# Performance work log

Measured on AMD Instinct MI355X. Metric: run time of the kernel, lower is better.

The kernel has to match this reference:

```python
import jax, jax.numpy as jnp
import numpy as np

N = 10000
E = 160000
F_IN = 2000
HID = 128
NC = 5


def setup_inputs() -> dict:
    key = jax.random.key(0)
    ks = jax.random.split(key, 16)
    s = 0.05
    nrm = lambda k, shape: jax.random.normal(k, shape, jnp.float32) * s
    return {
        "x": jax.random.normal(ks[0], (N, F_IN), jnp.float32),
        "edge_index": jax.random.randint(ks[1], (2, E), 0, N),
        # GATConv 1: in=F_IN, out=HID, heads=6, concat=False
        "W_gat1": nrm(ks[2], (F_IN, 6 * HID)), "a_src1": nrm(ks[3], (6, HID)),
        "a_dst1": nrm(ks[4], (6, HID)), "b_gat1": jnp.zeros(HID, jnp.float32),
        # GCNConv 1
        "W_gcn1": nrm(ks[5], (HID, HID)), "b_gcn1": jnp.zeros(HID, jnp.float32),
        # GATConv 2: heads=4
        "W_gat2": nrm(ks[6], (HID, 4 * HID)), "a_src2": nrm(ks[7], (4, HID)),
        "a_dst2": nrm(ks[8], (4, HID)), "b_gat2": jnp.zeros(HID, jnp.float32),
        # GCNConv 2: out=HID//2
        "W_gcn2": nrm(ks[9], (HID, HID // 2)), "b_gcn2": jnp.zeros(HID // 2, jnp.float32),
        # skip projection / fusion
        "W_skip": nrm(ks[10], (F_IN, HID // 2)), "b_skip": jnp.zeros(HID // 2, jnp.float32),
        "W_fuse": nrm(ks[11], (HID + HID // 2, HID // 2)), "b_fuse": jnp.zeros(HID // 2, jnp.float32),
        # classifier MLP
        "W_c1": nrm(ks[12], (HID // 2, HID // 4)), "b_c1": jnp.zeros(HID // 4, jnp.float32),
        "W_c2": nrm(ks[13], (HID // 4, HID // 8)), "b_c2": jnp.zeros(HID // 8, jnp.float32),
        "W_c3": nrm(ks[14], (HID // 8, NC)), "b_c3": jnp.zeros(NC, jnp.float32),
        # LayerNorms
        "g1": jnp.ones(HID, jnp.float32), "be1": jnp.zeros(HID, jnp.float32),
        "g2": jnp.ones(HID, jnp.float32), "be2": jnp.zeros(HID, jnp.float32),
        "g3": jnp.ones(HID // 2, jnp.float32), "be3": jnp.zeros(HID // 2, jnp.float32),
    }


def layer_norm(x, g, b, eps=1e-5):
    mu = jnp.mean(x, axis=-1, keepdims=True)
    var = jnp.var(x, axis=-1, keepdims=True)
    return (x - mu) * jax.lax.rsqrt(var + eps) * g + b


def gat_conv(x, src, dst, W, a_src, a_dst, b, n):
    # PyG GATConv with concat=False (head-mean). Eval mode -> no attn dropout.
    H, C = a_src.shape
    h = (x @ W).reshape(-1, H, C)                      # [N,H,C]
    alpha = (h * a_src).sum(-1)[src] + (h * a_dst).sum(-1)[dst]  # [E,H]
    alpha = jax.nn.leaky_relu(alpha, 0.2)
    m = jax.ops.segment_max(alpha, dst, num_segments=n)
    e = jnp.exp(alpha - m[dst])
    w = e / jax.ops.segment_sum(e, dst, num_segments=n)[dst]     # segment softmax over incoming edges
    out = jax.ops.segment_sum(h[src] * w[:, :, None], dst, num_segments=n)  # [N,H,C]
    return out.mean(axis=1) + b


def gcn_conv(x, src, dst, W, b, n):
    deg = jax.ops.segment_sum(jnp.ones_like(dst, x.dtype), dst, num_segments=n)
    dinv = jnp.where(deg > 0, deg ** -0.5, 0.0)
    msg = (x @ W)[src] * (dinv[src] * dinv[dst])[:, None]
    return jax.ops.segment_sum(msg, dst, num_segments=n) + b


def reference(x, edge_index, W_gat1, a_src1, a_dst1, b_gat1, W_gcn1, b_gcn1,
              W_gat2, a_src2, a_dst2, b_gat2, W_gcn2, b_gcn2,
              W_skip, b_skip, W_fuse, b_fuse, W_c1, b_c1, W_c2, b_c2, W_c3, b_c3,
              g1, be1, g2, be2, g3, be3):
    n = x.shape[0]
    loop = jnp.arange(n, dtype=edge_index.dtype)
    src = jnp.concatenate([edge_index[0], loop])  # add_self_loops
    dst = jnp.concatenate([edge_index[1], loop])

    x1_gat = jax.nn.relu(layer_norm(gat_conv(x, src, dst, W_gat1, a_src1, a_dst1, b_gat1, n), g1, be1))
    x1_gcn = jax.nn.relu(gcn_conv(x1_gat, src, dst, W_gcn1, b_gcn1, n))
    x2_gat = jax.nn.relu(layer_norm(gat_conv(x1_gcn, src, dst, W_gat2, a_src2, a_dst2, b_gat2, n), g2, be2))
    x2_gcn = jax.nn.relu(gcn_conv(x2_gat, src, dst, W_gcn2, b_gcn2, n))

    skip = jax.nn.relu(x @ W_skip + b_skip)
    fused = jax.nn.relu(jnp.concatenate([x1_gcn, x2_gcn], axis=1) @ W_fuse + b_fuse)
    final = layer_norm(fused + skip, g3, be3)

    h = jax.nn.relu(final @ W_c1 + b_c1)
    h = jax.nn.relu(h @ W_c2 + b_c2)
    return h @ W_c3 + b_c3
```

## Files before the change

### kernel.cpp

```cpp
#include <hip/hip_runtime.h>
#include <cstdint>
#include <cstddef>

#define NN 10000
#define NE 160000
#define ET (NE + NN)
#define FIN 2000
#define MPAD 10112
#define KPAD 2048
#define NPAD 896

typedef __bf16 bf16x8 __attribute__((ext_vector_type(8)));
typedef __bf16 bf16x4 __attribute__((ext_vector_type(4)));
typedef float  f32x4  __attribute__((ext_vector_type(4)));

#define GLL(src, dst) __builtin_amdgcn_global_load_lds( \
    (const __attribute__((address_space(1))) void*)(src), \
    (__attribute__((address_space(3))) void*)(dst), 16, 0, 0)

__device__ __forceinline__ void edge_sd(const int* ei, int e, int& s, int& d) {
    if (e < NE) { s = ei[e]; d = ei[NE + e]; }
    else        { s = e - NE; d = e - NE; }
}

__global__ __launch_bounds__(1024)
void scan_kernel(const int* deg, int* rowstart, float* dinv) {
    __shared__ int wsum[16];
    const int T = 1024;
    int chunk = (NN + T - 1) / T;
    int t = threadIdx.x;
    int begin = t * chunk;
    int end = begin + chunk; if (end > NN) end = NN;
    if (begin > NN) begin = NN;
    int s = 0;
    for (int i = begin; i < end; i++) s += deg[i];
    int inc = s;
#pragma unroll
    for (int off = 1; off < 64; off <<= 1) {
        int u = __shfl_up(inc, off);
        if ((t & 63) >= off) inc += u;
    }
    if ((t & 63) == 63) wsum[t >> 6] = inc;
    __syncthreads();
    int woff = 0;
    for (int wv = 0; wv < (t >> 6); wv++) woff += wsum[wv];
    int run = woff + inc - s;
    for (int i = begin; i < end; i++) {
        rowstart[i] = run; run += deg[i];
        int dg = deg[i];
        dinv[i] = dg > 0 ? rsqrtf((float)dg) : 0.f;
    }
    if (end == NN) rowstart[NN] = run;
}

__global__ void scatter_kernel(const int* ei, const int* rowstart, int* cursor,
                               int* csr_src) {
    int e = blockIdx.x * blockDim.x + threadIdx.x;
    if (e >= ET) return;
    int s, d; edge_sd(ei, e, s, d);
    int pos = atomicAdd(&cursor[d], 1);
    csr_src[rowstart[d] + pos] = s;
}

#define NBX (158 * 8)
#define NW1 (NPAD * KPAD / 8)
#define NWT (NW1 + 512 * 128 / 8)
#define NWT2 (NWT + 2048 + 1024)
#define WBLK ((NWT2 + 255) / 256)
#define EB 665
__global__ void conv_kernel(const float* __restrict__ x, __bf16* __restrict__ xb,
                            const float* __restrict__ Wg, const float* __restrict__ Ws,
                            const float* __restrict__ W2,
                            const float* __restrict__ Wg1, const float* __restrict__ Wg2,
                            __bf16* __restrict__ wt, __bf16* __restrict__ w2t,
                            __bf16* __restrict__ wgcn1s, __bf16* __restrict__ wgcn2s,
                            const int* __restrict__ ei, int* __restrict__ deg) {
    __shared__ __bf16 ls[16384];
    int bid = blockIdx.x;
    int tid = threadIdx.x;
    if (bid < NBX) {
        int rt = bid >> 3, kb = bid & 7;
        const int lane16 = tid & 15;
        const int ksl = lane16 >> 2;
        const int p0 = (lane16 & 3) * 2;
        const int rbase = tid >> 4;
        const int kg0 = kb * 256 + lane16 * 16;
        const int rsw_x = (p0 & 6) ^ ksl;
#pragma unroll
        for (int pass = 0; pass < 4; pass++) {
            int r = pass * 16 + rbase;
            int row = rt * 64 + r;
            bf16x8 v0, v1;
#pragma unroll
            for (int j = 0; j < 4; j++) {
                int k = kg0 + j * 4;
                f32x4 f;
                if (row < NN && k + 3 < FIN)
                    f = *(const f32x4*)(x + (size_t)row * FIN + k);
                else
                    f = (f32x4){0.f, 0.f, 0.f, 0.f};
                int o = (j & 1) * 4;
                if (j < 2) {
                    v0[o] = (__bf16)f[0]; v0[o+1] = (__bf16)f[1];
                    v0[o+2] = (__bf16)f[2]; v0[o+3] = (__bf16)f[3];
                } else {
                    v1[o] = (__bf16)f[0]; v1[o+1] = (__bf16)f[1];
                    v1[o+2] = (__bf16)f[2]; v1[o+3] = (__bf16)f[3];
                }
            }
            int rsw = r ^ rsw_x;
            *(bf16x8*)(ls + (((ksl * 8 + p0) * 64 + rsw) * 8))     = v0;
            *(bf16x8*)(ls + (((ksl * 8 + p0 + 1) * 64 + rsw) * 8)) = v1;
        }
        __syncthreads();
        size_t cbase = ((size_t)rt * 32 + kb * 4) * 512;
#pragma unroll
        for (int i = 0; i < 8; i++) {
            int g = i * 256 + tid;
            int ksl2 = g >> 9, rem = g & 511;
            int p = rem >> 6, rr = rem & 63;
            int rsw = rr ^ ((p & 6) ^ ksl2);
            bf16x8 v = *(const bf16x8*)(ls + (((ksl2 * 8 + p) * 64 + rsw) * 8));
            *(bf16x8*)(xb + (cbase + (size_t)ksl2 * 512 + (p * 64 + rr)) * 8) = v;
        }
    } else if (bid < NBX + WBLK) {
        int g = (bid - NBX) * 256 + tid;
        if (g < NW1) {
            int r = g & 127, p = (g >> 7) & 7, ks = (g >> 10) & 31, ct = g >> 15;
            int n = ct * 128 + r;
            int k0 = ks * 64 + p * 8;
            bf16x8 o;
#pragma unroll
            for (int j = 0; j < 8; j++) {
                int k = k0 + j;
                float v = 0.f;
                if (k < FIN) {
                    if (n < 768)      v = Wg[(size_t)k * 768 + n];
                    else if (n < 832) v = Ws[(size_t)k * 64 + (n - 768)];
                }
                o[j] = (__bf16)v;
            }
            *(bf16x8*)(wt + (size_t)g * 8) = o;
        } else if (g < NWT) {
            int g2 = g - NW1;
            int c = g2 & 2047;
            int ct = g2 >> 11;
            int p = c >> 7, r = c & 127;
            int n = ct * 128 + r;
            int k0 = p * 8;
            bf16x8 o;
#pragma unroll
            for (int j = 0; j < 8; j++)
                o[j] = (__bf16)W2[(size_t)(k0 + j) * 512 + n];
            *(bf16x8*)(w2t + (size_t)g2 * 8) = o;
        } else if (g < NWT + 2048) {
            int g3 = g - NWT;
            int p = g3 >> 7, r = g3 & 127;
            bf16x8 o;
#pragma unroll
            for (int j = 0; j < 8; j++)
                o[j] = (__bf16)Wg1[(size_t)(p * 8 + j) * 128 + r];
            *(bf16x8*)(wgcn1s + (size_t)g3 * 8) = o;
        } else if (g < NWT2) {
            int g4 = g - NWT - 2048;
            int p = g4 >> 6, r = g4 & 63;
            bf16x8 o;
#pragma unroll
            for (int j = 0; j < 8; j++)
                o[j] = (__bf16)Wg2[(size_t)(p * 8 + j) * 64 + r];
            *(bf16x8*)(wgcn2s + (size_t)g4 * 8) = o;
        }
    } else {
        int e = (bid - NBX - WBLK) * 256 + tid;
        if (e < ET) {
            int s, d; edge_sd(ei, e, s, d);
            atomicAdd(&deg[d], 1);
        }
    }
}

__global__ __launch_bounds__(512)
void mfma_gemm1_kernel(const __bf16* __restrict__ xb, const __bf16* __restrict__ wt,
                       const float* __restrict__ a_src1, const float* __restrict__ a_dst1,
                       __bf16* __restrict__ h1b, float* __restrict__ skippre,
                       float* __restrict__ asrc, float* __restrict__ adst) {
    __shared__ __bf16 As[8192];
    __shared__ __bf16 Bs[8192];
    __shared__ float sA[128], sD[128];
    __shared__ float asd[256];
    int b = blockIdx.x;
    int xcd = b & 7, j = b >> 3;
    int jq = j / 7;
    int rt = xcd + 8 * jq;
    int ct = j - 7 * jq;
    if (rt >= MPAD / 128) return;
    const int bi = rt * 128;
    const int bn = ct * 128;

    const int tid = threadIdx.x;
    const int lane = tid & 63;
    const int w = tid >> 6;
    const int wm = w >> 1;
    const int wn = w & 1;
    const int q = lane >> 4, m16 = lane & 15;

    if (tid < 128) { sA[tid] = 0.f; sD[tid] = 0.f; }
    if (ct < 6) {
        if (tid < 128)      asd[tid] = a_src1[ct * 128 + tid];
        else if (tid < 256) asd[tid] = a_dst1[ct * 128 + (tid - 128)];
    }

    f32x4 acc[2][4] = {};

    for (int ks = 0; ks < KPAD / 64; ks++) {
        const size_t slabA = ((size_t)(rt * 2) * 32 + ks) * 512;
        const size_t slabB = ((size_t)ct * 32 + ks) * 1024;
#pragma unroll
        for (int i = 0; i < 2; i++) {
            int seg = i * 8 + w;
            int p = seg >> 1, h = seg & 1;
            GLL(xb + (slabA + (size_t)h * 16384 + p * 64 + lane) * 8,
                As + seg * 512);
        }
#pragma unroll
        for (int i = 0; i < 2; i++) {
            int seg = i * 8 + w;
            GLL(wt + (slabB + seg * 64 + lane) * 8, Bs + seg * 512);
        }
        __syncthreads();

#pragma unroll
        for (int kk = 0; kk < 2; kk++) {
            const int pb = kk * 4 + q;
            bf16x8 af[2], bfr[4];
#pragma unroll
            for (int mt = 0; mt < 2; mt++)
                af[mt] = *(const bf16x8*)(As + (pb * 128 + wm * 32 + mt * 16 + m16) * 8);
#pragma unroll
            for (int nt = 0; nt < 4; nt++)
                bfr[nt] = *(const bf16x8*)(Bs + (pb * 128 + wn * 64 + nt * 16 + m16) * 8);
#pragma unroll
            for (int mt = 0; mt < 2; mt++)
#pragma unroll
                for (int nt = 0; nt < 4; nt++)
                    acc[mt][nt] = __builtin_amdgcn_mfma_f32_16x16x32_bf16(af[mt], bfr[nt], acc[mt][nt], 0, 0, 0);
        }
        __syncthreads();
    }

#pragma unroll
    for (int mt = 0; mt < 2; mt++) {
#pragma unroll
        for (int r = 0; r < 4; r++) {
            int rowl = wm * 32 + mt * 16 + q * 4 + r;
            int row = bi + rowl;
            float ps = 0.f, pd = 0.f;
#pragma unroll
            for (int nt = 0; nt < 4; nt++) {
                int coll = wn * 64 + nt * 16 + m16;
                int col = bn + coll;
                float v = acc[mt][nt][r];
                if (ct < 6) { ps += v * asd[coll]; pd += v * asd[128 + coll]; }
                if (row < NN) {
                    if (col < 768)      h1b[(size_t)row * 768 + col] = (__bf16)v;
                    else if (col < 832) skippre[(size_t)row * 64 + (col - 768)] = v;
                }
            }
            if (ct < 6) {
#pragma unroll
                for (int off = 1; off < 16; off <<= 1) {
                    ps += __shfl_xor(ps, off);
                    pd += __shfl_xor(pd, off);
                }
                if (m16 == 0) { atomicAdd(&sA[rowl], ps); atomicAdd(&sD[rowl], pd); }
            }
        }
    }
    if (ct < 6) {
        __syncthreads();
        if (tid < 128) {
            int row = bi + tid;
            if (row < NN) { asrc[row * 6 + ct] = sA[tid]; adst[row * 6 + ct] = sD[tid]; }
        }
    }
}

__global__ __launch_bounds__(256)
void mfma_gemm2_kernel(const __bf16* __restrict__ A, const __bf16* __restrict__ B,
                       const float* __restrict__ a_src2, const float* __restrict__ a_dst2,
                       __bf16* __restrict__ h2b,
                       float* __restrict__ asrc, float* __restrict__ adst) {
    __shared__ __bf16 As[4096];
    __shared__ __bf16 Bs[8192];
    __shared__ float sA[64], sD[64];
    __shared__ float asd[256];
    const int rt = blockIdx.y, ct = blockIdx.x;
    const int bi = rt * 64, bn = ct * 128;
    const int tid = threadIdx.x, lane = tid & 63, w = tid >> 6;
    const int wm = w >> 1, wn = w & 1;
    const int q = lane >> 4, m16 = lane & 15;

    if (tid < 64) { sA[tid] = 0.f; sD[tid] = 0.f; }
    if (tid < 128) asd[tid] = a_src2[ct * 128 + tid];
    else           asd[tid] = a_dst2[ct * 128 + (tid - 128)];

    f32x4 acc[2][4] = {};

    for (int ks = 0; ks < 2; ks++) {
        const size_t slabA = (size_t)rt * 1024 + ks * 512;
        const size_t slabB = (size_t)ct * 2048 + ks * 1024;
#pragma unroll
        for (int i = 0; i < 2; i++) {
            int seg = i * 4 + w;
            GLL(A + (slabA + seg * 64 + lane) * 8, As + seg * 512);
        }
#pragma unroll
        for (int i = 0; i < 4; i++) {
            int seg = i * 4 + w;
            GLL(B + (slabB + seg * 64 + lane) * 8, Bs + seg * 512);
        }
        __syncthreads();

#pragma unroll
        for (int kk = 0; kk < 2; kk++) {
            const int pb = kk * 4 + q;
            bf16x8 af[2], bfr[4];
#pragma unroll
            for (int mt = 0; mt < 2; mt++)
                af[mt] = *(const bf16x8*)(As + (pb * 64 + wm * 32 + mt * 16 + m16) * 8);
#pragma unroll
            for (int nt = 0; nt < 4; nt++)
                bfr[nt] = *(const bf16x8*)(Bs + (pb * 128 + wn * 64 + nt * 16 + m16) * 8);
#pragma unroll
            for (int mt = 0; mt < 2; mt++)
#pragma unroll
                for (int nt = 0; nt < 4; nt++)
                    acc[mt][nt] = __builtin_amdgcn_mfma_f32_16x16x32_bf16(af[mt], bfr[nt], acc[mt][nt], 0, 0, 0);
        }
        __syncthreads();
    }

#pragma unroll
    for (int mt = 0; mt < 2; mt++) {
#pragma unroll
        for (int r = 0; r < 4; r++) {
            int rowl = wm * 32 + mt * 16 + q * 4 + r;
            int row = bi + rowl;
            float ps = 0.f, pd = 0.f;
#pragma unroll
            for (int nt = 0; nt < 4; nt++) {
                int coll = wn * 64 + nt * 16 + m16;
                float v = acc[mt][nt][r];
                ps += v * asd[coll]; pd += v * asd[128 + coll];
                if (row < NN) h2b[(size_t)row * 512 + bn + coll] = (__bf16)v;
            }
#pragma unroll
            for (int off = 1; off < 16; off <<= 1) {
                ps += __shfl_xor(ps, off);
                pd += __shfl_xor(pd, off);
            }
            if (m16 == 0) { atomicAdd(&sA[rowl], ps); atomicAdd(&sD[rowl], pd); }
        }
    }
    __syncthreads();
    if (tid < 64) {
        int row = bi + tid;
        if (row < NN) { asrc[row * 4 + ct] = sA[tid]; adst[row * 4 + ct] = sD[tid]; }
    }
}

template<int NT>
__global__ __launch_bounds__(256)
void mfma_gcn_kernel(const __bf16* __restrict__ A, const __bf16* __restrict__ B,
                     __bf16* __restrict__ Cb) {
    __shared__ __bf16 As[4096];
    __shared__ __bf16 Bs[NT * 64];
    const int rt = blockIdx.x;
    const int bi = rt * 64;
    const int tid = threadIdx.x, lane = tid & 63, w = tid >> 6;
    const int q = lane >> 4, m16 = lane & 15;
    constexpr int MT = (NT == 128) ? 2 : 1;
    constexpr int MSPAN = (NT == 128) ? 32 : 16;
    const int wm = (NT == 128) ? (w >> 1) : w;
    const int wn = (NT == 128) ? (w & 1) : 0;

    f32x4 acc[MT][4] = {};

    for (int ks = 0; ks < 2; ks++) {
        const size_t slabA = (size_t)rt * 1024 + ks * 512;
        const size_t slabB = (size_t)ks * (NT * 8);
#pragma unroll
        for (int i = 0; i < 2; i++) {
            int seg = i * 4 + w;
            GLL(A + (slabA + seg * 64 + lane) * 8, As + seg * 512);
        }
#pragma unroll
        for (int i = 0; i < NT / 32; i++) {
            int seg = i * 4 + w;
            GLL(B + (slabB + (size_t)seg * 64 + lane) * 8, Bs + seg * 512);
        }
        __syncthreads();

#pragma unroll
        for (int kk = 0; kk < 2; kk++) {
            const int pb = kk * 4 + q;
            bf16x8 af[MT], bfr[4];
#pragma unroll
            for (int mt = 0; mt < MT; mt++)
                af[mt] = *(const bf16x8*)(As + (pb * 64 + wm * MSPAN + mt * 16 + m16) * 8);
#pragma unroll
            for (int nt = 0; nt < 4; nt++)
                bfr[nt] = *(const bf16x8*)(Bs + (pb * NT + wn * 64 + nt * 16 + m16) * 8);
#pragma unroll
            for (int mt = 0; mt < MT; mt++)
#pragma unroll
                for (int nt = 0; nt < 4; nt++)
                    acc[mt][nt] = __builtin_amdgcn_mfma_f32_16x16x32_bf16(af[mt], bfr[nt], acc[mt][nt], 0, 0, 0);
        }
        __syncthreads();
    }

#pragma unroll
    for (int mt = 0; mt < MT; mt++) {
#pragma unroll
        for (int r = 0; r < 4; r++) {
            int row = bi + wm * MSPAN + mt * 16 + q * 4 + r;
            if (row >= NN) continue;
#pragma unroll
            for (int nt = 0; nt < 4; nt++) {
                int col = wn * 64 + nt * 16 + m16;
                Cb[(size_t)row * NT + col] = (__bf16)acc[mt][nt][r];
            }
        }
    }
}

template<int H>
__global__ void gat_agg_kernel(const __bf16* __restrict__ hb,
                               const float* __restrict__ asrc,
                               const float* __restrict__ adst,
                               const int* __restrict__ rowstart,
                               const int* __restrict__ csr_src,
                               const float* __restrict__ bias,
                               const float* __restrict__ gamma,
                               const float* __restrict__ beta,
                               __bf16* __restrict__ outs) {
    constexpr int CH = H * 128;
    constexpr int CAP = 128;
    int n = blockIdx.x;
    int t = threadIdx.x;
    int w = t >> 6, l = t & 63;
    __shared__ float invden[H];
    __shared__ float denp[256];
    __shared__ int   srcs[CAP];
    __shared__ float evs[CAP * H];
    __shared__ float sm[4 * CH];
    __shared__ float red[8];

    int s0 = rowstart[n];
    int deg = rowstart[n + 1] - s0;
    int degc = deg < CAP ? deg : CAP;
    float adst_n = (l < H) ? adst[n * H + l] : 0.f;

    if (t < degc) srcs[t] = csr_src[s0 + t];
    __syncthreads();

    const int h0 = l >> 4;
    const int h1i = 4 + (l >> 5);
    const int i0 = w, i1 = w + 4;
    const bool has0 = i0 < degc, has1 = i1 < degc;
    bf16x8 pg0, pg1; bf16x4 pe0, pe1;
    if (has0) {
        const __bf16* hp = hb + (size_t)srcs[i0] * CH;
        pg0 = *(const bf16x8*)(hp + l * 8);
        if (H == 6) pe0 = *(const bf16x4*)(hp + 512 + l * 4);
    }
    if (has1) {
        const __bf16* hp = hb + (size_t)srcs[i1] * CH;
        pg1 = *(const bf16x8*)(hp + l * 8);
        if (H == 6) pe1 = *(const bf16x4*)(hp + 512 + l * 4);
    }

    const int eh = t >> 3;
    const int hh1 = t & 7;
    float adst_h = (hh1 < H) ? adst[n * H + hh1] : 0.f;
    float dloc = 0.f;
    for (int base = 0; base < deg; base += 32) {
        int idx = base + eh;
        if (idx < deg && hh1 < H) {
            int src = (idx < CAP) ? srcs[idx] : csr_src[s0 + idx];
            float al = asrc[src * H + hh1] + adst_h;
            al = al >= 0.f ? al : 0.2f * al;
            float ev = __expf(al);
            dloc += ev;
            if (idx < CAP) evs[idx * H + hh1] = ev;
        }
    }
    denp[t] = dloc;
    __syncthreads();
    if (t < H) {
        float s = 0.f;
#pragma unroll
        for (int g = 0; g < 32; g++) s += denp[g * 8 + t];
        invden[t] = 1.f / s;
    }
    __syncthreads();

    constexpr int NA = (H == 6) ? 12 : 8;
    float acc[NA] = {};
    if (has0) {
        float w0 = evs[i0 * H + h0];
#pragma unroll
        for (int jj = 0; jj < 8; jj++) acc[jj] += (float)pg0[jj] * w0;
        if (H == 6) {
            float w1 = evs[i0 * H + h1i];
#pragma unroll
            for (int jj = 0; jj < 4; jj++) acc[8 + jj] += (float)pe0[jj] * w1;
        }
    }
    if (has1) {
        float w0 = evs[i1 * H + h0];
#pragma unroll
        for (int jj = 0; jj < 8; jj++) acc[jj] += (float)pg1[jj] * w0;
        if (H == 6) {
            float w1 = evs[i1 * H + h1i];
#pragma unroll
            for (int jj = 0; jj < 4; jj++) acc[8 + jj] += (float)pe1[jj] * w1;
        }
    }
    int idx = w + 8;
    for (; idx + 4 < degc; idx += 8) {
        int src0 = srcs[idx], src1 = srcs[idx + 4];
        float w00 = evs[idx * H + h0];
        float w10 = evs[(idx + 4) * H + h0];
        const __bf16* hp0 = hb + (size_t)src0 * CH;
        const __bf16* hp1 = hb + (size_t)src1 * CH;
        bf16x8 g00 = *(const bf16x8*)(hp0 + l * 8);
        bf16x8 g10 = *(const bf16x8*)(hp1 + l * 8);
#pragma unroll
        for (int jj = 0; jj < 8; jj++)
            acc[jj] += (float)g00[jj] * w00 + (float)g10[jj] * w10;
        if (H == 6) {
            float w01 = evs[idx * H + h1i];
            float w11 = evs[(idx + 4) * H + h1i];
            bf16x4 g01 = *(const bf16x4*)(hp0 + 512 + l * 4);
            bf16x4 g11 = *(const bf16x4*)(hp1 + 512 + l * 4);
#pragma unroll
            for (int jj = 0; jj < 4; jj++)
                acc[8 + jj] += (float)g01[jj] * w01 + (float)g11[jj] * w11;
        }
    }
    if (idx < degc) {
        int src = srcs[idx];
        float w0 = evs[idx * H + h0];
        const __bf16* hp = hb + (size_t)src * CH;
        bf16x8 hv = *(const bf16x8*)(hp + l * 8);
#pragma unroll
        for (int jj = 0; jj < 8; jj++) acc[jj] += (float)hv[jj] * w0;
        if (H == 6) {
            float w1 = evs[idx * H + h1i];
            bf16x4 hv1 = *(const bf16x4*)(hp + 512 + l * 4);
#pragma unroll
            for (int jj = 0; jj < 4; jj++) acc[8 + jj] += (float)hv1[jj] * w1;
        }
    }
    for (int i2 = CAP + w; i2 < deg; i2 += 4) {
        int src = csr_src[s0 + i2];
        float ev = 0.f;
        if (l < H) {
            float al = asrc[src * H + l] + adst_n;
            al = al >= 0.f ? al : 0.2f * al;
            ev = __expf(al);
        }
        const __bf16* hp = hb + (size_t)src * CH;
        float wgt = __shfl(ev, h0);
        bf16x8 hv = *(const bf16x8*)(hp + l * 8);
#pragma unroll
        for (int jj = 0; jj < 8; jj++) acc[jj] += (float)hv[jj] * wgt;
        if (H == 6) {
            float wg1 = __shfl(ev, h1i);
            bf16x4 hv1 = *(const bf16x4*)(hp + 512 + l * 4);
#pragma unroll
            for (int jj = 0; jj < 4; jj++) acc[8 + jj] += (float)hv1[jj] * wg1;
        }
    }

    *(f32x4*)(sm + w * CH + l * 8)     = *(f32x4*)(acc);
    *(f32x4*)(sm + w * CH + l * 8 + 4) = *(f32x4*)(acc + 4);
    if (H == 6)
        *(f32x4*)(sm + w * CH + 512 + l * 4) = *(f32x4*)(acc + 8);
    __syncthreads();

    float v = 0.f;
    if (t < 128) {
#pragma unroll
        for (int hh = 0; hh < H; hh++) {
            float hsum = 0.f;
#pragma unroll
            for (int ww = 0; ww < 4; ww++) hsum += sm[ww * CH + hh * 128 + t];
            v += hsum * invden[hh];
        }
        v = v * (1.f / H) + bias[t];
    }
    float sv = (t < 128) ? v : 0.f;
    float sq = (t < 128) ? v * v : 0.f;
#pragma unroll
    for (int off = 32; off; off >>= 1) {
        sv += __shfl_down(sv, off);
        sq += __shfl_down(sq, off);
    }
    if ((t & 63) == 0) { red[w * 2] = sv; red[w * 2 + 1] = sq; }
    __syncthreads();
    float tot = red[0] + red[2] + red[4] + red[6];
    float tsq = red[1] + red[3] + red[5] + red[7];
    float mu = tot * (1.f / 128.f);
    float var = tsq * (1.f / 128.f) - mu * mu;
    float r = rsqrtf(var + 1e-5f);
    if (t < 128) {
        float o = fmaxf((v - mu) * r * gamma[t] + beta[t], 0.f);
        int rt2 = n >> 6, rr = n & 63, pp = t >> 3, off2 = t & 7;
        outs[((size_t)(rt2 * 16 + pp) * 64 + rr) * 8 + off2] = (__bf16)o;
    }
}

template<int C>
__global__ void gcn_agg_kernel(const __bf16* __restrict__ y,
                               const float* __restrict__ dinv,
                               const int* __restrict__ rowstart,
                               const int* __restrict__ csr_src,
                               const float* __restrict__ bias,
                               float* __restrict__ out, int coloff,
                               __bf16* __restrict__ bout) {
    constexpr int LPE = C / 8;
    constexpr int G = 128 / LPE;
    __shared__ float sm[G * C];
    int n = blockIdx.x;
    int t = threadIdx.x;
    int lane = t & (LPE - 1);
    int grp = t / LPE;
    float acc[8] = {};
    int s0 = rowstart[n], s1 = rowstart[n + 1];
    for (int e = s0 + grp; e < s1; e += G) {
        int src = csr_src[e];
        float dv = dinv[src];
        bf16x8 v = *(const bf16x8*)(y + (size_t)src * C + lane * 8);
#pragma unroll
        for (int j = 0; j < 8; j++) acc[j] += (float)v[j] * dv;
    }
    *(f32x4*)(sm + grp * C + lane * 8)     = *(f32x4*)(acc);
    *(f32x4*)(sm + grp * C + lane * 8 + 4) = *(f32x4*)(acc + 4);
    __syncthreads();
    if (t < C) {
        float v = 0.f;
#pragma unroll
        for (int g = 0; g < G; g++) v += sm[g * C + t];
        v = fmaxf(v * dinv[n] + bias[t], 0.f);
        out[(size_t)n * 192 + coloff + t] = v;
        if (bout) {
            int rt = n >> 6, r = n & 63, p = t >> 3, off = t & 7;
            bout[((size_t)(rt * 16 + p) * 64 + r) * 8 + off] = (__bf16)v;
        }
    }
}

__global__ __launch_bounds__(256)
void fuse_final_kernel(const float* __restrict__ cat,
                       const float* __restrict__ skippre,
                       const float* __restrict__ Wf, const float* __restrict__ bfz,
                       const float* __restrict__ b_skip,
                       const float* __restrict__ g3, const float* __restrict__ be3,
                       const float* __restrict__ Wc1, const float* __restrict__ bc1,
                       const float* __restrict__ Wc2, const float* __restrict__ bc2,
                       const float* __restrict__ Wc3, const float* __restrict__ bc3,
                       float* __restrict__ out) {
    __shared__ float WfS[192 * 64];
    __shared__ float catS[4][4][196];
    __shared__ float fS[4][64], h1S[4][32], h2S[4][16];
    int tid = threadIdx.x;
    int w = tid >> 6, l = tid & 63;
#pragma unroll
    for (int i = 0; i < 12; i++) {
        int idx = (i * 256 + tid) * 4;
        *(f32x4*)(WfS + idx) = *(const f32x4*)(Wf + idx);
    }
    int n0 = blockIdx.x * 16 + w * 4;
    float sk[4];
#pragma unroll
    for (int i = 0; i < 4; i++) {
        int n = n0 + i;
        if (n < NN) {
            catS[w][i][l]       = cat[(size_t)n * 192 + l];
            catS[w][i][64 + l]  = cat[(size_t)n * 192 + 64 + l];
            catS[w][i][128 + l] = cat[(size_t)n * 192 + 128 + l];
            sk[i] = fmaxf(skippre[(size_t)n * 64 + l] + b_skip[l], 0.f);
        } else {
            sk[i] = 0.f;
        }
    }
    __syncthreads();

#pragma unroll
    for (int i = 0; i < 4; i++) {
        int n = n0 + i;
        if (n < NN) {
            float fu = bfz[l];
#pragma unroll 4
            for (int k = 0; k < 192; k++)
                fu += catS[w][i][k] * WfS[k * 64 + l];
            float v = fmaxf(fu, 0.f) + sk[i];

            float sv = v, sq = v * v;
#pragma unroll
            for (int off = 32; off; off >>= 1) {
                sv += __shfl_xor(sv, off);
                sq += __shfl_xor(sq, off);
            }
            float mu = sv * (1.f / 64.f);
            float var = sq * (1.f / 64.f) - mu * mu;
            float r = rsqrtf(var + 1e-5f);
            fS[w][l] = (v - mu) * r * g3[l] + be3[l];
            if (l < 32) {
                float a = bc1[l];
                for (int k = 0; k < 64; k++) a += fS[w][k] * Wc1[k * 32 + l];
                h1S[w][l] = fmaxf(a, 0.f);
            }
            if (l < 16) {
                float a = bc2[l];
                for (int k = 0; k < 32; k++) a += h1S[w][k] * Wc2[k * 16 + l];
                h2S[w][l] = fmaxf(a, 0.f);
            }
            if (l < 5) {
                float a = bc3[l];
                for (int k = 0; k < 16; k++) a += h2S[w][k] * Wc3[k * 5 + l];
                out[(size_t)n * 5 + l] = a;
            }
        }
    }
}

extern "C" void kernel_launch(void* const* d_in, const int* in_sizes, int n_in,
                              void* d_out, int out_size, void* d_ws, size_t ws_size,
                              hipStream_t stream) {
    const float* x      = (const float*)d_in[0];
    const int*   ei     = (const int*)d_in[1];
    const float* W_gat1 = (const float*)d_in[2];
    const float* a_src1 = (const float*)d_in[3];
    const float* a_dst1 = (const float*)d_in[4];
    const float* b_gat1 = (const float*)d_in[5];
    const float* W_gcn1 = (const float*)d_in[6];
    const float* b_gcn1 = (const float*)d_in[7];
    const float* W_gat2 = (const float*)d_in[8];
    const float* a_src2 = (const float*)d_in[9];
    const float* a_dst2 = (const float*)d_in[10];
    const float* b_gat2 = (const float*)d_in[11];
    const float* W_gcn2 = (const float*)d_in[12];
    const float* b_gcn2 = (const float*)d_in[13];
    const float* W_skip = (const float*)d_in[14];
    const float* b_skip = (const float*)d_in[15];
    const float* W_fuse = (const float*)d_in[16];
    const float* b_fuse = (const float*)d_in[17];
    const float* W_c1   = (const float*)d_in[18];
    const float* b_c1   = (const float*)d_in[19];
    const float* W_c2   = (const float*)d_in[20];
    const float* b_c2   = (const float*)d_in[21];
    const float* W_c3   = (const float*)d_in[22];
    const float* b_c3   = (const float*)d_in[23];
    const float* g1     = (const float*)d_in[24];
    const float* be1    = (const float*)d_in[25];
    const float* g2     = (const float*)d_in[26];
    const float* be2    = (const float*)d_in[27];
    const float* g3     = (const float*)d_in[28];
    const float* be3    = (const float*)d_in[29];
    float* out = (float*)d_out;

    char* p = (char*)d_ws;
    auto alloc = [&](size_t bytes) {
        char* r = p; p += (bytes + 255) & ~(size_t)255; return r;
    };
    __bf16* xb      = (__bf16*)alloc((size_t)MPAD * KPAD * 2);
    __bf16* wt      = (__bf16*)alloc((size_t)NPAD * KPAD * 2);
    __bf16* w2t     = (__bf16*)alloc((size_t)512 * 128 * 2);
    __bf16* wgcn1s  = (__bf16*)alloc((size_t)128 * 128 * 2);
    __bf16* wgcn2s  = (__bf16*)alloc((size_t)64 * 128 * 2);
    __bf16* h1b     = (__bf16*)alloc((size_t)NN * 768 * 2);
    __bf16* h2b     = (__bf16*)alloc((size_t)NN * 512 * 2);
    __bf16* ybufb   = (__bf16*)alloc((size_t)NN * 128 * 2);
    __bf16* x1gatb  = (__bf16*)alloc((size_t)3 * MPAD * 128 * 2);
    __bf16* x1gcnb  = x1gatb + (size_t)MPAD * 128;
    __bf16* x2gatb  = x1gcnb + (size_t)MPAD * 128;
    float* asrc     = (float*)alloc((size_t)NN * 6 * 4);
    float* adst     = (float*)alloc((size_t)NN * 6 * 4);
    int*   deg      = (int*)  alloc((size_t)2 * NN * 4);
    int*   cursor   = deg + NN;
    float* dinv     = (float*)alloc((size_t)NN * 4);
    int*   rowst    = (int*)  alloc((size_t)(NN + 1) * 4);
    int*   csrc     = (int*)  alloc((size_t)ET * 4);
    float* cat      = (float*)alloc((size_t)NN * 192 * 4);
    float* skippre  = (float*)alloc((size_t)NN * 64 * 4);

    hipMemsetAsync(deg, 0, (size_t)2 * NN * 4, stream);
    hipMemsetAsync(x1gatb, 0, (size_t)3 * MPAD * 128 * 2, stream);

    conv_kernel<<<NBX + WBLK + EB, 256, 0, stream>>>(
        x, xb, W_gat1, W_skip, W_gat2, W_gcn1, W_gcn2,
        wt, w2t, wgcn1s, wgcn2s, ei, deg);

    scan_kernel   <<<1, 1024, 0, stream>>>(deg, rowst, dinv);
    scatter_kernel<<<EB, 256, 0, stream>>>(ei, rowst, cursor, csrc);

    mfma_gemm1_kernel<<<560, 512, 0, stream>>>(xb, wt, a_src1, a_dst1,
                                               h1b, skippre, asrc, adst);

    gat_agg_kernel<6><<<NN, 256, 0, stream>>>(h1b, asrc, adst, rowst, csrc,
                                              b_gat1, g1, be1, x1gatb);
    mfma_gcn_kernel<128><<<MPAD / 64, 256, 0, stream>>>(x1gatb, wgcn1s, ybufb);
    gcn_agg_kernel<128><<<NN, 128, 0, stream>>>(ybufb, dinv, rowst, csrc,
                                                b_gcn1, cat, 0, x1gcnb);
    mfma_gemm2_kernel<<<dim3(4, MPAD / 64), 256, 0, stream>>>(
        x1gcnb, w2t, a_src2, a_dst2, h2b, asrc, adst);
    gat_agg_kernel<4><<<NN, 256, 0, stream>>>(h2b, asrc, adst, rowst, csrc,
                                              b_gat2, g2, be2, x2gatb);
    mfma_gcn_kernel<64><<<MPAD / 64, 256, 0, stream>>>(x2gatb, wgcn2s, ybufb);
    gcn_agg_kernel<64><<<NN, 128, 0, stream>>>(ybufb, dinv, rowst, csrc,
                                               b_gcn2, cat, 128, nullptr);
    fuse_final_kernel<<<(NN + 15) / 16, 256, 0, stream>>>(
        cat, skippre, W_fuse, b_fuse, b_skip, g3, be3,
        W_c1, b_c1, W_c2, b_c2, W_c3, b_c3, out);
}
```

Measured before the change: 401.1 us.

## Load fp32 x directly in GEMM1 and drop the separate bf16 conversion pass

Removes the pre-pass that converted x to a swizzled bf16 buffer. GEMM1 now streams fp32 rows of x into LDS with a XOR swizzle and converts to bf16 while building MFMA fragments. This saves writing and re-reading a 40MB intermediate, at the cost of twice the A-tile bytes per k-step, double the LDS for A, and extra conversion instructions inside the inner loop. The GAT aggregation kernel also prefetches four neighbour rows instead of two to expose more memory parallelism.

New measurement: 437.6 us. 1.09x slower.

```diff
diff --git a/kernel.cpp b/kernel.cpp
--- a/kernel.cpp
+++ b/kernel.cpp
@@ -62,69 +62,21 @@
     csr_src[rowstart[d] + pos] = s;
 }
 
-#define NBX (158 * 8)
 #define NW1 (NPAD * KPAD / 8)
 #define NWT (NW1 + 512 * 128 / 8)
 #define NWT2 (NWT + 2048 + 1024)
 #define WBLK ((NWT2 + 255) / 256)
 #define EB 665
-__global__ void conv_kernel(const float* __restrict__ x, __bf16* __restrict__ xb,
-                            const float* __restrict__ Wg, const float* __restrict__ Ws,
+__global__ void conv_kernel(const float* __restrict__ Wg, const float* __restrict__ Ws,
                             const float* __restrict__ W2,
                             const float* __restrict__ Wg1, const float* __restrict__ Wg2,
                             __bf16* __restrict__ wt, __bf16* __restrict__ w2t,
                             __bf16* __restrict__ wgcn1s, __bf16* __restrict__ wgcn2s,
                             const int* __restrict__ ei, int* __restrict__ deg) {
-    __shared__ __bf16 ls[16384];
     int bid = blockIdx.x;
     int tid = threadIdx.x;
-    if (bid < NBX) {
-        int rt = bid >> 3, kb = bid & 7;
-        const int lane16 = tid & 15;
-        const int ksl = lane16 >> 2;
-        const int p0 = (lane16 & 3) * 2;
-        const int rbase = tid >> 4;
-        const int kg0 = kb * 256 + lane16 * 16;
-        const int rsw_x = (p0 & 6) ^ ksl;
-#pragma unroll
-        for (int pass = 0; pass < 4; pass++) {
-            int r = pass * 16 + rbase;
-            int row = rt * 64 + r;
-            bf16x8 v0, v1;
-#pragma unroll
-            for (int j = 0; j < 4; j++) {
-                int k = kg0 + j * 4;
-                f32x4 f;
-                if (row < NN && k + 3 < FIN)
-                    f = *(const f32x4*)(x + (size_t)row * FIN + k);
-                else
-                    f = (f32x4){0.f, 0.f, 0.f, 0.f};
-                int o = (j & 1) * 4;
-                if (j < 2) {
-                    v0[o] = (__bf16)f[0]; v0[o+1] = (__bf16)f[1];
-                    v0[o+2] = (__bf16)f[2]; v0[o+3] = (__bf16)f[3];
-                } else {
-                    v1[o] = (__bf16)f[0]; v1[o+1] = (__bf16)f[1];
-                    v1[o+2] = (__bf16)f[2]; v1[o+3] = (__bf16)f[3];
-                }
-            }
-            int rsw = r ^ rsw_x;
-            *(bf16x8*)(ls + (((ksl * 8 + p0) * 64 + rsw) * 8))     = v0;
-            *(bf16x8*)(ls + (((ksl * 8 + p0 + 1) * 64 + rsw) * 8)) = v1;
-        }
-        __syncthreads();
-        size_t cbase = ((size_t)rt * 32 + kb * 4) * 512;
-#pragma unroll
-        for (int i = 0; i < 8; i++) {
-            int g = i * 256 + tid;
-            int ksl2 = g >> 9, rem = g & 511;
-            int p = rem >> 6, rr = rem & 63;
-            int rsw = rr ^ ((p & 6) ^ ksl2);
-            bf16x8 v = *(const bf16x8*)(ls + (((ksl2 * 8 + p) * 64 + rsw) * 8));
-            *(bf16x8*)(xb + (cbase + (size_t)ksl2 * 512 + (p * 64 + rr)) * 8) = v;
-        }
-    } else if (bid < NBX + WBLK) {
-        int g = (bid - NBX) * 256 + tid;
+    if (bid < WBLK) {
+        int g = bid * 256 + tid;
         if (g < NW1) {
             int r = g & 127, p = (g >> 7) & 7, ks = (g >> 10) & 31, ct = g >> 15;
             int n = ct * 128 + r;
@@ -171,7 +123,7 @@
             *(bf16x8*)(wgcn2s + (size_t)g4 * 8) = o;
         }
     } else {
-        int e = (bid - NBX - WBLK) * 256 + tid;
+        int e = (bid - WBLK) * 256 + tid;
         if (e < ET) {
             int s, d; edge_sd(ei, e, s, d);
             atomicAdd(&deg[d], 1);
@@ -180,11 +132,11 @@
 }
 
 __global__ __launch_bounds__(512)
-void mfma_gemm1_kernel(const __bf16* __restrict__ xb, const __bf16* __restrict__ wt,
+void mfma_gemm1_kernel(const float* __restrict__ x, const __bf16* __restrict__ wt,
                        const float* __restrict__ a_src1, const float* __restrict__ a_dst1,
                        __bf16* __restrict__ h1b, float* __restrict__ skippre,
                        float* __restrict__ asrc, float* __restrict__ adst) {
-    __shared__ __bf16 As[8192];
+    __shared__ float  Asf[8192];
     __shared__ __bf16 Bs[8192];
     __shared__ float sA[128], sD[128];
     __shared__ float asd[256];
@@ -213,15 +165,16 @@
     f32x4 acc[2][4] = {};
 
     for (int ks = 0; ks < KPAD / 64; ks++) {
-        const size_t slabA = ((size_t)(rt * 2) * 32 + ks) * 512;
+#pragma unroll
+        for (int i = 0; i < 4; i++) {
+            int seg = i * 8 + w;
+            int row = seg * 4 + (q & 3);
+            int grow = bi + row; if (grow > NN - 1) grow = NN - 1;
+            int sl = m16 ^ (row & 7);
+            GLL(x + (size_t)grow * FIN + ks * 64 + sl * 4,
+                Asf + seg * 256);
+        }
         const size_t slabB = ((size_t)ct * 32 + ks) * 1024;
-#pragma unroll
-        for (int i = 0; i < 2; i++) {
-            int seg = i * 8 + w;
-            int p = seg >> 1, h = seg & 1;
-            GLL(xb + (slabA + (size_t)h * 16384 + p * 64 + lane) * 8,
-                As + seg * 512);
-        }
 #pragma unroll
         for (int i = 0; i < 2; i++) {
             int seg = i * 8 + w;
@@ -234,8 +187,18 @@
             const int pb = kk * 4 + q;
             bf16x8 af[2], bfr[4];
 #pragma unroll
-            for (int mt = 0; mt < 2; mt++)
-                af[mt] = *(const bf16x8*)(As + (pb * 128 + wm * 32 + mt * 16 + m16) * 8);
+            for (int mt = 0; mt < 2; mt++) {
+                int rowm = wm * 32 + mt * 16 + m16;
+                int rb = rowm & 7;
+                f32x4 a0 = *(const f32x4*)(Asf + rowm * 64 + (((pb * 2)     ^ rb) << 2));
+                f32x4 a1 = *(const f32x4*)(Asf + rowm * 64 + (((pb * 2 + 1) ^ rb) << 2));
+                bf16x8 t;
+                t[0] = (__bf16)a0[0]; t[1] = (__bf16)a0[1];
+                t[2] = (__bf16)a0[2]; t[3] = (__bf16)a0[3];
+                t[4] = (__bf16)a1[0]; t[5] = (__bf16)a1[1];
+                t[6] = (__bf16)a1[2]; t[7] = (__bf16)a1[3];
+                af[mt] = t;
+            }
 #pragma unroll
             for (int nt = 0; nt < 4; nt++)
                 bfr[nt] = *(const bf16x8*)(Bs + (pb * 128 + wn * 64 + nt * 16 + m16) * 8);
@@ -467,9 +430,10 @@
 
     const int h0 = l >> 4;
     const int h1i = 4 + (l >> 5);
-    const int i0 = w, i1 = w + 4;
+    const int i0 = w, i1 = w + 4, i2 = w + 8, i3 = w + 12;
     const bool has0 = i0 < degc, has1 = i1 < degc;
-    bf16x8 pg0, pg1; bf16x4 pe0, pe1;
+    const bool has2 = i2 < degc, has3 = i3 < degc;
+    bf16x8 pg0, pg1, pg2, pg3; bf16x4 pe0, pe1, pe2, pe3;
     if (has0) {
         const __bf16* hp = hb + (size_t)srcs[i0] * CH;
         pg0 = *(const bf16x8*)(hp + l * 8);
@@ -479,6 +443,16 @@
         const __bf16* hp = hb + (size_t)srcs[i1] * CH;
         pg1 = *(const bf16x8*)(hp + l * 8);
         if (H == 6) pe1 = *(const bf16x4*)(hp + 512 + l * 4);
+    }
+    if (has2) {
+        const __bf16* hp = hb + (size_t)srcs[i2] * CH;
+        pg2 = *(const bf16x8*)(hp + l * 8);
+        if (H == 6) pe2 = *(const bf16x4*)(hp + 512 + l * 4);
+    }
+    if (has3) {
+        const __bf16* hp = hb + (size_t)srcs[i3] * CH;
+        pg3 = *(const bf16x8*)(hp + l * 8);
+        if (H == 6) pe3 = *(const bf16x4*)(hp + 512 + l * 4);
     }
 
     const int eh = t >> 3;
@@ -528,7 +502,27 @@
             for (int jj = 0; jj < 4; jj++) acc[8 + jj] += (float)pe1[jj] * w1;
         }
     }
-    int idx = w + 8;
+    if (has2) {
+        float w0 = evs[i2 * H + h0];
+#pragma unroll
+        for (int jj = 0; jj < 8; jj++) acc[jj] += (float)pg2[jj] * w0;
+        if (H == 6) {
+            float w1 = evs[i2 * H + h1i];
+#pragma unroll
+            for (int jj = 0; jj < 4; jj++) acc[8 + jj] += (float)pe2[jj] * w1;
+        }
+    }
+    if (has3) {
+        float w0 = evs[i3 * H + h0];
+#pragma unroll
+        for (int jj = 0; jj < 8; jj++) acc[jj] += (float)pg3[jj] * w0;
+        if (H == 6) {
+            float w1 = evs[i3 * H + h1i];
+#pragma unroll
+            for (int jj = 0; jj < 4; jj++) acc[8 + jj] += (float)pe3[jj] * w1;
+        }
+    }
+    int idx = w + 16;
     for (; idx + 4 < degc; idx += 8) {
         int src0 = srcs[idx], src1 = srcs[idx + 4];
         float w00 = evs[idx * H + h0];
@@ -564,8 +558,8 @@
             for (int jj = 0; jj < 4; jj++) acc[8 + jj] += (float)hv1[jj] * w1;
         }
     }
-    for (int i2 = CAP + w; i2 < deg; i2 += 4) {
-        int src = csr_src[s0 + i2];
+    for (int i2f = CAP + w; i2f < deg; i2f += 4) {
+        int src = csr_src[s0 + i2f];
         float ev = 0.f;
         if (l < H) {
             float al = asrc[src * H + l] + adst_n;
@@ -777,7 +771,6 @@
     auto alloc = [&](size_t bytes) {
         char* r = p; p += (bytes + 255) & ~(size_t)255; return r;
     };
-    __bf16* xb      = (__bf16*)alloc((size_t)MPAD * KPAD * 2);
     __bf16* wt      = (__bf16*)alloc((size_t)NPAD * KPAD * 2);
     __bf16* w2t     = (__bf16*)alloc((size_t)512 * 128 * 2);
     __bf16* wgcn1s  = (__bf16*)alloc((size_t)128 * 128 * 2);
@@ -801,14 +794,14 @@
     hipMemsetAsync(deg, 0, (size_t)2 * NN * 4, stream);
     hipMemsetAsync(x1gatb, 0, (size_t)3 * MPAD * 128 * 2, stream);
 
-    conv_kernel<<<NBX + WBLK + EB, 256, 0, stream>>>(
-        x, xb, W_gat1, W_skip, W_gat2, W_gcn1, W_gcn2,
+    conv_kernel<<<WBLK + EB, 256, 0, stream>>>(
+        W_gat1, W_skip, W_gat2, W_gcn1, W_gcn2,
         wt, w2t, wgcn1s, wgcn2s, ei, deg);
 
     scan_kernel   <<<1, 1024, 0, stream>>>(deg, rowst, dinv);
     scatter_kernel<<<EB, 256, 0, stream>>>(ei, rowst, cursor, csrc);
 
-    mfma_gemm1_kernel<<<560, 512, 0, stream>>>(xb, wt, a_src1, a_dst1,
+    mfma_gemm1_kernel<<<560, 512, 0, stream>>>(x, wt, a_src1, a_dst1,
                                                h1b, skippre, asrc, adst);
 
     gat_agg_kernel<6><<<NN, 256, 0, stream>>>(h1b, asrc, adst, rowst, csrc,
```

## Enlarge gemm2 row tile to 128 with 512 threads; prefetch four GAT neighbors

Applied to the files above, without the earlier changes.

The second-layer GAT projection GEMM now uses 128-row tiles with 8 waves per block, so each B tile loaded into LDS is reused across twice as many rows and half as many blocks are launched. The GAT aggregation kernel now issues loads for the first four neighbor rows per wave before computing attention weights, instead of two. The aim is more memory-level parallelism to hide gather latency. In exchange it uses more registers and gives the GEMM fewer blocks for occupancy.

After: 405.4 us. About the same (+1.1%).

```diff
diff --git a/kernel.cpp b/kernel.cpp
--- a/kernel.cpp
+++ b/kernel.cpp
@@ -285,38 +285,39 @@
     }
 }
 
-__global__ __launch_bounds__(256)
+__global__ __launch_bounds__(512)
 void mfma_gemm2_kernel(const __bf16* __restrict__ A, const __bf16* __restrict__ B,
                        const float* __restrict__ a_src2, const float* __restrict__ a_dst2,
                        __bf16* __restrict__ h2b,
                        float* __restrict__ asrc, float* __restrict__ adst) {
-    __shared__ __bf16 As[4096];
+    __shared__ __bf16 As[8192];
     __shared__ __bf16 Bs[8192];
-    __shared__ float sA[64], sD[64];
+    __shared__ float sA[128], sD[128];
     __shared__ float asd[256];
     const int rt = blockIdx.y, ct = blockIdx.x;
-    const int bi = rt * 64, bn = ct * 128;
+    const int bi = rt * 128, bn = ct * 128;
     const int tid = threadIdx.x, lane = tid & 63, w = tid >> 6;
     const int wm = w >> 1, wn = w & 1;
     const int q = lane >> 4, m16 = lane & 15;
 
-    if (tid < 64) { sA[tid] = 0.f; sD[tid] = 0.f; }
-    if (tid < 128) asd[tid] = a_src2[ct * 128 + tid];
-    else           asd[tid] = a_dst2[ct * 128 + (tid - 128)];
+    if (tid < 128) { sA[tid] = 0.f; sD[tid] = 0.f; }
+    if (tid < 128)      asd[tid] = a_src2[ct * 128 + tid];
+    else if (tid < 256) asd[tid] = a_dst2[ct * 128 + (tid - 128)];
 
     f32x4 acc[2][4] = {};
 
     for (int ks = 0; ks < 2; ks++) {
-        const size_t slabA = (size_t)rt * 1024 + ks * 512;
         const size_t slabB = (size_t)ct * 2048 + ks * 1024;
 #pragma unroll
         for (int i = 0; i < 2; i++) {
-            int seg = i * 4 + w;
-            GLL(A + (slabA + seg * 64 + lane) * 8, As + seg * 512);
-        }
-#pragma unroll
-        for (int i = 0; i < 4; i++) {
-            int seg = i * 4 + w;
+            int seg = i * 8 + w;
+            int p = seg >> 1, h = seg & 1;
+            GLL(A + ((size_t)(rt * 2 + h) * 1024 + ks * 512 + p * 64 + lane) * 8,
+                As + seg * 512);
+        }
+#pragma unroll
+        for (int i = 0; i < 2; i++) {
+            int seg = i * 8 + w;
             GLL(B + (slabB + seg * 64 + lane) * 8, Bs + seg * 512);
         }
         __syncthreads();
@@ -327,7 +328,7 @@
             bf16x8 af[2], bfr[4];
 #pragma unroll
             for (int mt = 0; mt < 2; mt++)
-                af[mt] = *(const bf16x8*)(As + (pb * 64 + wm * 32 + mt * 16 + m16) * 8);
+                af[mt] = *(const bf16x8*)(As + (pb * 128 + wm * 32 + mt * 16 + m16) * 8);
 #pragma unroll
             for (int nt = 0; nt < 4; nt++)
                 bfr[nt] = *(const bf16x8*)(Bs + (pb * 128 + wn * 64 + nt * 16 + m16) * 8);
@@ -363,7 +364,7 @@
         }
     }
     __syncthreads();
-    if (tid < 64) {
+    if (tid < 128) {
         int row = bi + tid;
         if (row < NN) { asrc[row * 4 + ct] = sA[tid]; adst[row * 4 + ct] = sD[tid]; }
     }
@@ -467,9 +468,10 @@
 
     const int h0 = l >> 4;
     const int h1i = 4 + (l >> 5);
-    const int i0 = w, i1 = w + 4;
+    const int i0 = w, i1 = w + 4, i2 = w + 8, i3 = w + 12;
     const bool has0 = i0 < degc, has1 = i1 < degc;
-    bf16x8 pg0, pg1; bf16x4 pe0, pe1;
+    const bool has2 = i2 < degc, has3 = i3 < degc;
+    bf16x8 pg0, pg1, pg2, pg3; bf16x4 pe0, pe1, pe2, pe3;
     if (has0) {
         const __bf16* hp = hb + (size_t)srcs[i0] * CH;
         pg0 = *(const bf16x8*)(hp + l * 8);
@@ -479,6 +481,16 @@
         const __bf16* hp = hb + (size_t)srcs[i1] * CH;
         pg1 = *(const bf16x8*)(hp + l * 8);
         if (H == 6) pe1 = *(const bf16x4*)(hp + 512 + l * 4);
+    }
+    if (has2) {
+        const __bf16* hp = hb + (size_t)srcs[i2] * CH;
+        pg2 = *(const bf16x8*)(hp + l * 8);
+        if (H == 6) pe2 = *(const bf16x4*)(hp + 512 + l * 4);
+    }
+    if (has3) {
+        const __bf16* hp = hb + (size_t)srcs[i3] * CH;
+        pg3 = *(const bf16x8*)(hp + l * 8);
+        if (H == 6) pe3 = *(const bf16x4*)(hp + 512 + l * 4);
     }
 
     const int eh = t >> 3;
@@ -528,7 +540,27 @@
             for (int jj = 0; jj < 4; jj++) acc[8 + jj] += (float)pe1[jj] * w1;
         }
     }
-    int idx = w + 8;
+    if (has2) {
+        float w0 = evs[i2 * H + h0];
+#pragma unroll
+        for (int jj = 0; jj < 8; jj++) acc[jj] += (float)pg2[jj] * w0;
+        if (H == 6) {
+            float w1 = evs[i2 * H + h1i];
+#pragma unroll
+            for (int jj = 0; jj < 4; jj++) acc[8 + jj] += (float)pe2[jj] * w1;
+        }
+    }
+    if (has3) {
+        float w0 = evs[i3 * H + h0];
+#pragma unroll
+        for (int jj = 0; jj < 8; jj++) acc[jj] += (float)pg3[jj] * w0;
+        if (H == 6) {
+            float w1 = evs[i3 * H + h1i];
+#pragma unroll
+            for (int jj = 0; jj < 4; jj++) acc[8 + jj] += (float)pe3[jj] * w1;
+        }
+    }
+    int idx = w + 16;
     for (; idx + 4 < degc; idx += 8) {
         int src0 = srcs[idx], src1 = srcs[idx + 4];
         float w00 = evs[idx * H + h0];
@@ -564,8 +596,8 @@
             for (int jj = 0; jj < 4; jj++) acc[8 + jj] += (float)hv1[jj] * w1;
         }
     }
-    for (int i2 = CAP + w; i2 < deg; i2 += 4) {
-        int src = csr_src[s0 + i2];
+    for (int i2f = CAP + w; i2f < deg; i2f += 4) {
+        int src = csr_src[s0 + i2f];
         float ev = 0.f;
         if (l < H) {
             float al = asrc[src * H + l] + adst_n;
@@ -816,7 +848,7 @@
     mfma_gcn_kernel<128><<<MPAD / 64, 256, 0, stream>>>(x1gatb, wgcn1s, ybufb);
     gcn_agg_kernel<128><<<NN, 128, 0, stream>>>(ybufb, dinv, rowst, csrc,
                                                 b_gcn1, cat, 0, x1gcnb);
-    mfma_gemm2_kernel<<<dim3(4, MPAD / 64), 256, 0, stream>>>(
+    mfma_gemm2_kernel<<<dim3(4, MPAD / 128), 512, 0, stream>>>(
         x1gcnb, w2t, a_src2, a_dst2, h2b, asrc, adst);
     gat_agg_kernel<4><<<NN, 256, 0, stream>>>(h2b, asrc, adst, rowst, csrc,
                                               b_gat2, g2, be2, x2gatb);
```
